# Optimization experiments

Measured on AMD Instinct MI355X. Metric: run time of the kernel, lower is better.

Reference implementation:

```python
import jax, jax.numpy as jnp
import numpy as np

LS = (0, 2, 4, 6, 8)
L_IN, L_OUT, SYM = 8, 8, 2
A, B, N, C = 2, 2, 1024, 8  # ti_n, te_n, voxels, b_out

def _triples():
    out = []
    for l in range(0, L_OUT + 1, SYM):
        for l1 in range(0, L_IN + 1, SYM):
            for l2 in range(l1, L_IN + 1, SYM):
                if abs(l2 - l1) <= l <= l1 + l2:
                    out.append((l, l1, l2))
    return tuple(out)

TRIPLES = _triples()
# Clebsch-Gordan-like constants (fixed random; same structural shapes as the real CG tables)
_rng = np.random.RandomState(42)
CG_R = {t: jnp.asarray((_rng.randn(2 * t[0] + 1, 2 * t[1] + 1, 2 * t[2] + 1) * 0.1).astype(np.float32)) for t in TRIPLES}
CG_L = {t: jnp.asarray((_rng.randn(2 * t[0] + 1, 2 * t[2] + 1, 2 * t[1] + 1) * 0.1).astype(np.float32)) for t in TRIPLES}


def setup_inputs() -> dict:
    key = jax.random.key(0)
    ks = jax.random.split(key, 11)
    inp = {}
    for i, l in enumerate(LS):
        i_l = 5 if l == 0 else 2
        inp[f"x{l}"] = jax.random.normal(ks[i], (A, B, N, i_l, 2 * l + 1), dtype=jnp.float32)
        inp[f"w{l}"] = jax.random.uniform(ks[5 + i], (A, B, i_l, C, 2 * l + 1), dtype=jnp.float32) * 0.1
    inp["bias"] = jnp.zeros((A, B, 1, C, 1, 1), dtype=jnp.float32)
    return inp


def _forward(x0, x2, x4, x6, x8, w0, w2, w4, w6, w8, bias):
    xs = {0: x0, 2: x2, 4: x4, 6: x6, 8: x8}
    ws = {0: w0, 2: w2, 4: w4, 6: w6, 8: w8}
    # spectral convolution: rh[l] = x[l] @ w[l], shape (a,b,n,c,2l+1,2l+1)
    rh = {}
    for l in LS:
        r = jnp.einsum('abnil,abiok->abnolk', xs[l], ws[l])
        if l == 0:
            r = r + bias
        rh[l] = r
    # CG tensor-product quadratic nonlinearity
    rh_n = {}
    for (l, l1, l2) in TRIPLES:
        a, b, n, c = rh[l1].shape[:4]
        xx = jnp.einsum('abncij,klj->abnckli', rh[l2], CG_R[(l, l1, l2)])
        xx = xx.reshape(a, b, n, c, 2 * l + 1, -1)  # flat dim = (2l1+1)*(2l2+1)
        yy = jnp.einsum('abncji,klj->abnckil', rh[l1], CG_L[(l, l1, l2)])
        yy = yy.reshape(a, b, n, c, 2 * l + 1, -1)
        z = jnp.einsum('abncki,abncji->abnckj', yy, xx)  # (a,b,n,c,2l+1,2l+1)
        rh_n[l] = z if l not in rh_n else rh_n[l] + z
    # power-spectrum features
    feats = []
    for l in LS:
        n_l = np.float32(8.0 * np.pi ** 2 / (2 * l + 1))
        f = jnp.sum(rh_n[l] ** 2, axis=(4, 5)).reshape(A, B, -1)  # (a,b,n*c)
        feats.append(n_l * f)
    feats = jnp.concatenate(feats, axis=2)  # (a,b, 5*n*c)
    return feats, rh_n


def reference(x0, x2, x4, x6, x8, w0, w2, w4, w6, w8, bias):
    feats, rh_n = _forward(x0, x2, x4, x6, x8, w0, w2, w4, w6, w8, bias)
    return (feats, rh_n[0], rh_n[2], rh_n[4], rh_n[6], rh_n[8])
```

## Files before the change

kernel.cpp:

```cpp
#include <hip/hip_runtime.h>
#include <cmath>
#include <cstdint>
#include <vector>
#include <cstdlib>
#include <algorithm>

#define WGB 256

typedef float vf4 __attribute__((ext_vector_type(4)));

struct TripleMeta { int l,l1,l2,d,d1,d2,form,dp4,cgR,cgL,uv; };
struct AllMeta { TripleMeta t[48]; int nT, cgTotal, uvTotal; };

constexpr AllMeta build_meta() {
  AllMeta M{};
  const int LSl[5] = {0,2,4,6,8};
  int k=0, cg=0;
  for (int a=0;a<5;a++){ const int l=LSl[a];
    for (int b=0;b<5;b++){ const int l1=LSl[b];
      for (int l2=l1;l2<=8;l2+=2){
        if (!((l2-l1)<=l && l<=(l1+l2))) continue;
        TripleMeta m{};
        m.l=l; m.l1=l1; m.l2=l2;
        m.d=2*l+1; m.d1=2*l1+1; m.d2=2*l2+1;
        m.form = (l1==0) ? ((l2==0)?2:1) : 0;
        m.dp4 = ((m.d+3)/4)*4;
        m.cgR = cg; cg += m.d*m.d1*m.d2;
        M.t[k] = m; k++;
      } } }
  M.nT=k; M.cgTotal=cg;
  int cgl=cg;
  for (int i=0;i<k;i++){ M.t[i].cgL=cgl; cgl += M.t[i].d*M.t[i].d1*M.t[i].d2; }
  int uv=0;
  for (int i=0;i<k;i++){
    if (M.t[i].form==0){ M.t[i].uv=uv; uv += 4*M.t[i].dp4; }
    else if (M.t[i].form==1){ M.t[i].uv=uv; uv += 2*M.t[i].dp4; }
  }
  M.uvTotal=uv;
  return M;
}

constexpr AllMeta META_H = build_meta();
static_assert(META_H.nT==42, "nT");
static_assert(META_H.cgTotal==52334, "cgTotal");
static_assert(META_H.uvTotal==2048, "uvTotal");

__device__ constexpr AllMeta META = build_meta();

constexpr int CG_TOTAL  = 52334;
constexpr int UVS       = 2048;
constexpr int ZTOT      = 4520;
constexpr int NUC       = 417;
constexpr int XBS       = 104;

__device__ constexpr int DL[5]     = {1,5,9,13,17};
__device__ constexpr int T0G[6]    = {0,5,13,23,33,42};
__device__ constexpr int RHNB[5]   = {163840,196608,1015808,3670016,9207808};
__device__ constexpr int CBASE[5]  = {352,312,240,136,0};
__device__ constexpr int ZB[5]     = {0,8,208,856,2208};
__device__ constexpr int LEN5[5]   = {8,200,648,1352,2312};
__device__ constexpr int C4[6]     = {0,2,52,214,552,1130};

__global__ __launch_bounds__(128) void s2_prep(
    const float* __restrict__ w2, const float* __restrict__ w4,
    const float* __restrict__ w6, const float* __restrict__ w8,
    const float* __restrict__ cg, float* __restrict__ V)
{
  __shared__ float Rs[4928];
  const int bid = blockIdx.x;
  const int t   = bid >> 5;
  const int abc = bid & 31;
  const auto &m = META.t[t];
  if (m.form == 2) return;
  const int ab = abc >> 3, c = abc & 7;
  const int sz = m.d * m.d1 * m.d2;
  for (int i = threadIdx.x; i < sz; i += 128) Rs[i] = cg[m.cgR + i];
  __syncthreads();
  const float* ws[4] = {w2,w4,w6,w8};
  const int nout = (m.form==0 ? 4 : 2) * m.d;
  if ((int)threadIdx.x < nout){
    const int pq = threadIdx.x / m.d;
    const int k2 = threadIdx.x - pq*m.d;
    float s = 0.f;
    if (m.form==0){
      const int p = pq>>1, q = pq&1;
      const float* wA = ws[(m.l1>>1)-1] + ((ab*2+p)*8 + c)*m.d1;
      const float* wB = ws[(m.l2>>1)-1] + ((ab*2+q)*8 + c)*m.d2;
      const float* Rk = Rs + k2*m.d1*m.d2;
      for (int a=0;a<m.d1;a++){
        float t2 = 0.f;
        for (int j=0;j<m.d2;j++) t2 += wB[j]*Rk[a*m.d2+j];
        s += wA[a]*t2;
      }
    } else {
      const float* wB = ws[(m.l2>>1)-1] + ((ab*2+pq)*8 + c)*m.d2;
      const float* Rk = Rs + k2*m.d2;
      for (int j=0;j<m.d2;j++) s += wB[j]*Rk[j];
    }
    V[abc*UVS + m.uv + pq*m.dp4 + k2] = s;
  }
}

template<int D1>
__device__ __forceinline__ void u_itemA(const float* __restrict__ Lp, const float* xb,
    float* Ush, int dst, int dstr, int xo1, int xo2, int d2)
{
  float x0r[2*D1], x1r[2*D1];
  #pragma unroll
  for (int j=0;j<2*D1;j++){ x0r[j] = xb[xo1+j]; x1r[j] = xb[XBS+xo1+j]; }
  float a00=0.f,a01=0.f,a10=0.f,a11=0.f;
  float b00=0.f,b01=0.f,b10=0.f,b11=0.f;
  for (int b=0;b<d2;b++){
    float i00=0.f, i01=0.f, i10=0.f, i11=0.f;
    const float* Lb = Lp + b*D1;
    #pragma unroll
    for (int j=0;j<D1;j++){
      const float lv=Lb[j];
      i00+=lv*x0r[j]; i01+=lv*x0r[D1+j];
      i10+=lv*x1r[j]; i11+=lv*x1r[D1+j];
    }
    const float q00=xb[xo2+b],     q01=xb[xo2+d2+b];
    const float q10=xb[XBS+xo2+b], q11=xb[XBS+xo2+d2+b];
    a00+=q00*i00; a01+=q01*i00; a10+=q00*i01; a11+=q01*i01;
    b00+=q10*i10; b01+=q11*i10; b10+=q10*i11; b11+=q11*i11;
  }
  Ush[dst]=a00; Ush[dst+dstr]=a01; Ush[dst+2*dstr]=a10; Ush[dst+3*dstr]=a11;
  Ush[UVS+dst]=b00; Ush[UVS+dst+dstr]=b01; Ush[UVS+dst+2*dstr]=b10; Ush[UVS+dst+3*dstr]=b11;
}

__device__ __forceinline__ void u_item(const int4 w, const float* __restrict__ cg,
                                       const float* xb, float* Ush)
{
  const float* Lp = cg + w.x;
  const int dst = w.y & 0xFFFF, dstr = ((unsigned)w.y) >> 16;
  const int xo1 = w.z & 0xFF, xo2 = (w.z>>8)&0xFF;
  const int d1 = (w.z>>16)&0x3F, d2 = ((unsigned)w.z)>>22;
  if (d1 == 0){
    float a0=0.f, a1=0.f, b0=0.f, b1=0.f;
    for (int b=0;b<d2;b++){
      const float lv=Lp[b];
      a0+=lv*xb[xo2+b];     a1+=lv*xb[xo2+d2+b];
      b0+=lv*xb[XBS+xo2+b]; b1+=lv*xb[XBS+xo2+d2+b];
    }
    Ush[dst]=a0; Ush[dst+dstr]=a1;
    Ush[UVS+dst]=b0; Ush[UVS+dst+dstr]=b1;
    return;
  }
  switch(d1){
    case 5:  u_itemA<5>(Lp,xb,Ush,dst,dstr,xo1,xo2,d2); break;
    case 9:  u_itemA<9>(Lp,xb,Ush,dst,dstr,xo1,xo2,d2); break;
    case 13: u_itemA<13>(Lp,xb,Ush,dst,dstr,xo1,xo2,d2); break;
    default: u_itemA<17>(Lp,xb,Ush,dst,dstr,xo1,xo2,d2); break;
  }
}

template<int LI>
__device__ __forceinline__ float col_work(int k2, float rh0c, float c000,
    const float* __restrict__ Vc, const float* Ush,
    float* zsh, int zb)
{
  constexpr int d   = (LI==0)?1:(LI==1)?5:(LI==2)?9:(LI==3)?13:17;
  constexpr int np4 = (d+3)/4;
  float4 za[np4];
  #pragma unroll
  for (int i=0;i<np4;i++) za[i] = make_float4(0.f,0.f,0.f,0.f);
  #pragma unroll
  for (int t=T0G[LI]; t<T0G[LI+1]; t++){
    const auto &m = META.t[t];
    if (m.form==2){
      za[0].x += rh0c*rh0c*c000;
    } else {
      const int npr = (m.form==0)?4:2;
      #pragma unroll
      for (int pr=0;pr<npr;pr++){
        float v = Vc[m.uv + pr*m.dp4 + k2];
        if (m.form==1) v *= rh0c;
        const float4* Up = reinterpret_cast<const float4*>(Ush + m.uv + pr*m.dp4);
        #pragma unroll
        for (int rr=0;rr<np4;rr++){
          float4 u = Up[rr];
          za[rr].x += u.x*v; za[rr].y += u.y*v; za[rr].z += u.z*v; za[rr].w += u.w*v;
        }
      }
    }
  }
  float s = 0.f;
  #pragma unroll
  for (int rr=0;rr<np4;rr++){
    const float vals[4] = {za[rr].x, za[rr].y, za[rr].z, za[rr].w};
    #pragma unroll
    for (int e=0;e<4;e++){
      const int k1 = 4*rr+e;
      if (k1 < d){
        zsh[zb + k1*d + k2] = vals[e];
        s += vals[e]*vals[e];
      }
    }
  }
  return s;
}

__global__ __launch_bounds__(WGB,4) void s2_main(
    const float* __restrict__ x0, const float* __restrict__ x2, const float* __restrict__ x4,
    const float* __restrict__ x6, const float* __restrict__ x8,
    const float* __restrict__ w0, const float* __restrict__ bias,
    const float* __restrict__ cg, const int4* __restrict__ wiU,
    const float* __restrict__ V, float* __restrict__ out, float c000)
{
  __shared__ alignas(16) float SH[ZTOT + 2*UVS];
  __shared__ float xb[2*XBS];
  __shared__ float rh0s[16];
  __shared__ float fpart[360];
  const int tid = threadIdx.x;
  const int bid = blockIdx.x;
  const int ab  = bid >> 9;
  float* Ush = SH + ZTOT;

  {
    const int v  = tid >> 7;
    const int t2 = tid & 127;
    const int vox = bid*2 + v;
    float* xv = xb + v*XBS;
    if (t2 < 5)        xv[t2]           = x0[vox*5  + t2];
    else if (t2 < 15)  xv[8  + (t2-5)]  = x2[vox*10 + (t2-5)];
    else if (t2 < 33)  xv[18 + (t2-15)] = x4[vox*18 + (t2-15)];
    else if (t2 < 59)  xv[36 + (t2-33)] = x6[vox*26 + (t2-33)];
    else if (t2 < 93)  xv[62 + (t2-59)] = x8[vox*34 + (t2-59)];
    else if (t2 >= 96 && t2 < 104) {
      const int c = t2 - 96;
      float s = bias[ab*8 + c];
      for (int i=0;i<5;i++) s += x0[vox*5+i] * w0[(ab*5+i)*8 + c];
      rh0s[v*8 + c] = s;
    }
  }
  __syncthreads();

  u_item(wiU[tid], cg, xb, Ush);
  {
    const int r = NUC-1-tid;
    if (r >= WGB) u_item(wiU[r], cg, xb, Ush);
  }
  __syncthreads();

  const float* Vab = V + (ab*8)*UVS;
  #pragma unroll
  for (int v=0; v<2; v++){
    const int bid2 = bid*2 + v;
    const float* Uv = Ush + v*UVS;
    for (int col=tid; col<360; col+=WGB){
      int li, c, k2;
      if (col < 136)      { li=4; c = col/17;            k2 = col - c*17; }
      else if (col < 240) { const int r=col-136; li=3; c=r/13; k2=r-c*13; }
      else if (col < 312) { const int r=col-240; li=2; c=r/9;  k2=r-c*9;  }
      else if (col < 352) { const int r=col-312; li=1; c=r/5;  k2=r-c*5;  }
      else                { li=0; c=col-352; k2=0; }
      const int d = DL[li];
      const float rh0c = rh0s[v*8 + c];
      const float* Vc = Vab + c*UVS;
      const int zb = ZB[li] + c*d*d;
      float s;
      switch(li){
        case 4:  s = col_work<4>(k2, rh0c, c000, Vc, Uv, SH, zb); break;
        case 3:  s = col_work<3>(k2, rh0c, c000, Vc, Uv, SH, zb); break;
        case 2:  s = col_work<2>(k2, rh0c, c000, Vc, Uv, SH, zb); break;
        case 1:  s = col_work<1>(k2, rh0c, c000, Vc, Uv, SH, zb); break;
        default: s = col_work<0>(k2, rh0c, c000, Vc, Uv, SH, zb); break;
      }
      fpart[col] = s;
    }
    __syncthreads();

    for (int i4 = tid; i4 < 1130; i4 += WGB){
      int li;
      if      (i4 < C4[1]) li = 0;
      else if (i4 < C4[2]) li = 1;
      else if (i4 < C4[3]) li = 2;
      else if (i4 < C4[4]) li = 3;
      else                 li = 4;
      const int r4 = i4 - C4[li];
      const vf4 zv = *reinterpret_cast<const vf4*>(SH + ZB[li] + 4*r4);
      __builtin_nontemporal_store(zv, reinterpret_cast<vf4*>(out + RHNB[li] + bid2*LEN5[li] + 4*r4));
    }

    if (tid < 40){
      const int li = tid >> 3, c = tid & 7;
      const int d = DL[li];
      float s = 0.f;
      for (int k2=0;k2<d;k2++) s += fpart[CBASE[li] + c*d + k2];
      const double nl_d = 8.0*3.14159265358979323846*3.14159265358979323846/(double)(2*(2*li)+1);
      const int n = bid2 & 1023;
      __builtin_nontemporal_store((float)nl_d * s, out + ab*40960 + li*8192 + n*8 + c);
    }
    if (v==0) __syncthreads();
  }
}

namespace {

struct MTRng {
  uint32_t mt[624]; int mti;
  bool has_g; double g;
  void seed(uint32_t s){
    for (int pos=0; pos<624; pos++){ mt[pos]=s; s = 1812433253u*(s^(s>>30)) + (uint32_t)pos + 1u; }
    mti = 624; has_g=false; g=0.0;
  }
  uint32_t next32(){
    if (mti >= 624){
      for (int i=0;i<624;i++){
        uint32_t y = (mt[i]&0x80000000u) | (mt[(i+1)%624]&0x7fffffffu);
        mt[i] = mt[(i+397)%624] ^ (y>>1) ^ ((y&1u) ? 0x9908b0dfu : 0u);
      }
      mti = 0;
    }
    uint32_t y = mt[mti++];
    y ^= y>>11; y ^= (y<<7)&0x9d2c5680u; y ^= (y<<15)&0xefc60000u; y ^= y>>18;
    return y;
  }
  double rk_double(){
    uint32_t a = next32()>>5, b = next32()>>6;
    return (a*67108864.0 + b)/9007199254740992.0;
  }
  double gauss(){
    if (has_g){ has_g=false; return g; }
    double f,x1,x2,r2;
    do {
      x1 = 2.0*rk_double()-1.0;
      x2 = 2.0*rk_double()-1.0;
      r2 = x1*x1 + x2*x2;
    } while (r2 >= 1.0 || r2 == 0.0);
    f = std::sqrt(-2.0*std::log(r2)/r2);
    g = f*x1; has_g = true;
    return f*x2;
  }
};

constexpr int XOFS_H[5] = {0,8,18,36,62};

struct DeviceSetup {
  float* d_cg  = nullptr;
  float* d_v   = nullptr;
  int4*  d_wiU = nullptr;
  float  c000  = 0.f;
  DeviceSetup(){
    std::vector<float> h(2*CG_TOTAL);
    MTRng r; r.seed(42u);
    for (int i=0;i<2*CG_TOTAL;i++) h[i] = (float)(r.gauss()*0.1);
    c000 = h[META_H.t[0].cgL] * h[META_H.t[0].cgR];

    std::vector<std::pair<int,int4>> tmp;
    for (int t=0;t<META_H.nT;t++){
      const TripleMeta &m = META_H.t[t];
      if (m.form==0){
        const int xo1 = XOFS_H[m.l1>>1], xo2 = XOFS_H[m.l2>>1];
        for (int k1=0;k1<m.d;k1++){
          int4 e;
          e.x = m.cgL + k1*m.d1*m.d2;
          e.y = (m.uv + k1) | (m.dp4<<16);
          e.z = xo1 | (xo2<<8) | (m.d1<<16) | (m.d2<<22);
          e.w = 0;
          tmp.push_back({m.d2*(2*m.d1+4), e});
        }
      } else if (m.form==1){
        const int xo2 = XOFS_H[m.l2>>1];
        for (int k1=0;k1<m.d;k1++){
          int4 e;
          e.x = m.cgL + k1*m.d2;
          e.y = (m.uv + k1) | (m.dp4<<16);
          e.z = (xo2<<8) | (0<<16) | (m.d2<<22);
          e.w = 0;
          tmp.push_back({2*m.d2, e});
        }
      }
    }
    if ((int)tmp.size() != NUC) std::abort();
    std::stable_sort(tmp.begin(), tmp.end(),
                     [](const std::pair<int,int4>&a, const std::pair<int,int4>&b){
                       return a.first > b.first; });
    std::vector<int4> wiU(NUC);
    for (int i=0;i<NUC;i++) wiU[i] = tmp[i].second;

    (void)hipMalloc((void**)&d_cg,  sizeof(float)*2*CG_TOTAL);
    (void)hipMalloc((void**)&d_v,   sizeof(float)*32*UVS);
    (void)hipMalloc((void**)&d_wiU, sizeof(int4)*NUC);
    (void)hipMemcpy(d_cg,  h.data(),    sizeof(float)*2*CG_TOTAL, hipMemcpyHostToDevice);
    (void)hipMemcpy(d_wiU, wiU.data(),  sizeof(int4)*NUC,  hipMemcpyHostToDevice);
  }
};
DeviceSetup g_dev;

}

extern "C" void kernel_launch(void* const* d_in, const int* in_sizes, int n_in,
                              void* d_out, int out_size, void* d_ws, size_t ws_size,
                              hipStream_t stream)
{
  (void)in_sizes; (void)n_in; (void)d_ws; (void)ws_size; (void)out_size;
  const float* x0   = (const float*)d_in[0];
  const float* w0   = (const float*)d_in[1];
  const float* x2   = (const float*)d_in[2];
  const float* w2   = (const float*)d_in[3];
  const float* x4   = (const float*)d_in[4];
  const float* w4   = (const float*)d_in[5];
  const float* x6   = (const float*)d_in[6];
  const float* w6   = (const float*)d_in[7];
  const float* x8   = (const float*)d_in[8];
  const float* w8   = (const float*)d_in[9];
  const float* bias = (const float*)d_in[10];
  float* out = (float*)d_out;

  s2_prep<<<dim3(42*32), dim3(128), 0, stream>>>(w2,w4,w6,w8, g_dev.d_cg, g_dev.d_v);
  s2_main<<<dim3(2048), dim3(WGB), 0, stream>>>(x0,x2,x4,x6,x8, w0, bias,
                                                g_dev.d_cg, g_dev.d_wiU,
                                                g_dev.d_v, out, g_dev.c000);
}
```

Measured before the change: 249.1 us.

## Drop LDS staging of z, schedule per-wave work by degree, regroup prep blocks

The main kernel no longer stages the rh_n output tiles in shared memory. Each thread now writes its z column straight to global memory with nontemporal stores, and the two voxel passes and their barriers are merged into one. Cutting the LDS footprint allows the launch bound to rise to 8 workgroups per CU. Column work and U-item work are assigned to waves through static, degree-grouped schedules so each wave runs a single template instantiation and stays uniform. The prep kernel is also reorganised into 84 blocks of 512 threads instead of 1344 small blocks. The trade-off is that the strided scalar global stores are less coalesced than the earlier vectorised float4 stores from shared memory.

```diff
diff --git a/kernel.cpp b/kernel.cpp
--- a/kernel.cpp
+++ b/kernel.cpp
@@ -6,8 +6,6 @@
 #include <algorithm>
 
 #define WGB 256
-
-typedef float vf4 __attribute__((ext_vector_type(4)));
 
 struct TripleMeta { int l,l1,l2,d,d1,d2,form,dp4,cgR,cgL,uv; };
 struct AllMeta { TripleMeta t[48]; int nT, cgTotal, uvTotal; };
@@ -49,38 +47,46 @@
 
 constexpr int CG_TOTAL  = 52334;
 constexpr int UVS       = 2048;
-constexpr int ZTOT      = 4520;
-constexpr int NUC       = 417;
 constexpr int XBS       = 104;
+constexpr int WI_N      = 512;
 
 __device__ constexpr int DL[5]     = {1,5,9,13,17};
 __device__ constexpr int T0G[6]    = {0,5,13,23,33,42};
 __device__ constexpr int RHNB[5]   = {163840,196608,1015808,3670016,9207808};
 __device__ constexpr int CBASE[5]  = {352,312,240,136,0};
-__device__ constexpr int ZB[5]     = {0,8,208,856,2208};
 __device__ constexpr int LEN5[5]   = {8,200,648,1352,2312};
-__device__ constexpr int C4[6]     = {0,2,52,214,552,1130};
-
-__global__ __launch_bounds__(128) void s2_prep(
+
+__device__ constexpr int SCHED3[4][5][2] = {
+  {{4,0},{4,64},{3,0},{-1,0},{-1,0}},
+  {{4,128},{4,192},{3,64},{-1,0},{-1,0}},
+  {{4,256},{3,128},{2,0},{1,0},{-1,0}},
+  {{3,192},{2,64},{2,128},{1,64},{0,0}},
+};
+
+__global__ __launch_bounds__(512) void s2_prep(
     const float* __restrict__ w2, const float* __restrict__ w4,
     const float* __restrict__ w6, const float* __restrict__ w8,
     const float* __restrict__ cg, float* __restrict__ V)
 {
   __shared__ float Rs[4928];
-  const int bid = blockIdx.x;
-  const int t   = bid >> 5;
-  const int abc = bid & 31;
+  const int t    = blockIdx.x >> 1;
+  const int half = blockIdx.x & 1;
   const auto &m = META.t[t];
   if (m.form == 2) return;
-  const int ab = abc >> 3, c = abc & 7;
   const int sz = m.d * m.d1 * m.d2;
-  for (int i = threadIdx.x; i < sz; i += 128) Rs[i] = cg[m.cgR + i];
+  for (int i = threadIdx.x; i < sz; i += 512) Rs[i] = cg[m.cgR + i];
   __syncthreads();
   const float* ws[4] = {w2,w4,w6,w8};
-  const int nout = (m.form==0 ? 4 : 2) * m.d;
-  if ((int)threadIdx.x < nout){
-    const int pq = threadIdx.x / m.d;
-    const int k2 = threadIdx.x - pq*m.d;
+  const int npq  = (m.form==0) ? 4 : 2;
+  const int nout = npq * m.d;
+  const int tot  = 16 * nout;
+  for (int idx = threadIdx.x; idx < tot; idx += 512){
+    const int al  = idx / nout;
+    const int rem = idx - al*nout;
+    const int abc = half*16 + al;
+    const int ab = abc >> 3, c = abc & 7;
+    const int pq = rem / m.d;
+    const int k2 = rem - pq*m.d;
     float s = 0.f;
     if (m.form==0){
       const int p = pq>>1, q = pq&1;
@@ -131,6 +137,7 @@
 __device__ __forceinline__ void u_item(const int4 w, const float* __restrict__ cg,
                                        const float* xb, float* Ush)
 {
+  if (w.z == 0) return;
   const float* Lp = cg + w.x;
   const int dst = w.y & 0xFFFF, dstr = ((unsigned)w.y) >> 16;
   const int xo1 = w.z & 0xFF, xo2 = (w.z>>8)&0xFF;
@@ -156,10 +163,9 @@
 
 template<int LI>
 __device__ __forceinline__ float col_work(int k2, float rh0c, float c000,
-    const float* __restrict__ Vc, const float* Ush,
-    float* zsh, int zb)
-{
-  constexpr int d   = (LI==0)?1:(LI==1)?5:(LI==2)?9:(LI==3)?13:17;
+    const float* __restrict__ Vc, const float* Ush, float* __restrict__ zg)
+{
+  constexpr int d   = 4*LI + 1;
   constexpr int np4 = (d+3)/4;
   float4 za[np4];
   #pragma unroll
@@ -192,7 +198,7 @@
     for (int e=0;e<4;e++){
       const int k1 = 4*rr+e;
       if (k1 < d){
-        zsh[zb + k1*d + k2] = vals[e];
+        __builtin_nontemporal_store(vals[e], zg + k1*d);
         s += vals[e]*vals[e];
       }
     }
@@ -200,21 +206,38 @@
   return s;
 }
 
-__global__ __launch_bounds__(WGB,4) void s2_main(
+template<int LI>
+__device__ __forceinline__ void do_pass(int base, int lane, int bid,
+    const float* __restrict__ Vab, const float* Ush, const float* rh0s,
+    float* fpart, float* __restrict__ out, float c000)
+{
+  constexpr int d = 4*LI + 1;
+  const int col = base + lane;
+  if (col >= 16*d) return;
+  const int v  = (col >= 8*d) ? 1 : 0;
+  const int r  = col - v*8*d;
+  const int c  = r / d;
+  const int k2 = r - c*d;
+  float* zg = out + RHNB[LI] + (bid*2+v)*LEN5[LI] + c*(d*d) + k2;
+  const float s = col_work<LI>(k2, rh0s[v*8+c], c000, Vab + c*UVS, Ush + v*UVS, zg);
+  fpart[v*360 + CBASE[LI] + c*d + k2] = s;
+}
+
+__global__ __launch_bounds__(WGB,8) void s2_main(
     const float* __restrict__ x0, const float* __restrict__ x2, const float* __restrict__ x4,
     const float* __restrict__ x6, const float* __restrict__ x8,
     const float* __restrict__ w0, const float* __restrict__ bias,
     const float* __restrict__ cg, const int4* __restrict__ wiU,
     const float* __restrict__ V, float* __restrict__ out, float c000)
 {
-  __shared__ alignas(16) float SH[ZTOT + 2*UVS];
-  __shared__ float xb[2*XBS];
-  __shared__ float rh0s[16];
-  __shared__ float fpart[360];
+  __shared__ alignas(16) float SH[2*UVS + 2*XBS + 16 + 720];
+  float* const Ush   = SH;
+  float* const xb    = SH + 2*UVS;
+  float* const rh0s  = SH + 2*UVS + 2*XBS;
+  float* const fpart = SH + 2*UVS + 2*XBS + 16;
   const int tid = threadIdx.x;
   const int bid = blockIdx.x;
   const int ab  = bid >> 9;
-  float* Ush = SH + ZTOT;
 
   {
     const int v  = tid >> 7;
@@ -235,63 +258,38 @@
   }
   __syncthreads();
 
-  u_item(wiU[tid], cg, xb, Ush);
-  {
-    const int r = NUC-1-tid;
-    if (r >= WGB) u_item(wiU[r], cg, xb, Ush);
-  }
+  #pragma unroll 1
+  for (int it=0; it<2; it++) u_item(wiU[it*WGB + tid], cg, xb, Ush);
   __syncthreads();
 
   const float* Vab = V + (ab*8)*UVS;
-  #pragma unroll
-  for (int v=0; v<2; v++){
+  const int wid = tid>>6, lane = tid&63;
+  #pragma unroll 1
+  for (int pi=0; pi<5; pi++){
+    const int li = SCHED3[wid][pi][0];
+    if (li < 0) break;
+    const int base = SCHED3[wid][pi][1];
+    switch(li){
+      case 4:  do_pass<4>(base,lane,bid,Vab,Ush,rh0s,fpart,out,c000); break;
+      case 3:  do_pass<3>(base,lane,bid,Vab,Ush,rh0s,fpart,out,c000); break;
+      case 2:  do_pass<2>(base,lane,bid,Vab,Ush,rh0s,fpart,out,c000); break;
+      case 1:  do_pass<1>(base,lane,bid,Vab,Ush,rh0s,fpart,out,c000); break;
+      default: do_pass<0>(base,lane,bid,Vab,Ush,rh0s,fpart,out,c000); break;
+    }
+  }
+  __syncthreads();
+
+  if (tid < 80){
+    const int v  = (tid >= 40) ? 1 : 0;
+    const int r  = tid - v*40;
+    const int li = r >> 3, c = r & 7;
+    const int d = DL[li];
+    float s = 0.f;
+    for (int k2=0;k2<d;k2++) s += fpart[v*360 + CBASE[li] + c*d + k2];
+    const double nl_d = 8.0*3.14159265358979323846*3.14159265358979323846/(double)(2*(2*li)+1);
     const int bid2 = bid*2 + v;
-    const float* Uv = Ush + v*UVS;
-    for (int col=tid; col<360; col+=WGB){
-      int li, c, k2;
-      if (col < 136)      { li=4; c = col/17;            k2 = col - c*17; }
-      else if (col < 240) { const int r=col-136; li=3; c=r/13; k2=r-c*13; }
-      else if (col < 312) { const int r=col-240; li=2; c=r/9;  k2=r-c*9;  }
-      else if (col < 352) { const int r=col-312; li=1; c=r/5;  k2=r-c*5;  }
-      else                { li=0; c=col-352; k2=0; }
-      const int d = DL[li];
-      const float rh0c = rh0s[v*8 + c];
-      const float* Vc = Vab + c*UVS;
-      const int zb = ZB[li] + c*d*d;
-      float s;
-      switch(li){
-        case 4:  s = col_work<4>(k2, rh0c, c000, Vc, Uv, SH, zb); break;
-        case 3:  s = col_work<3>(k2, rh0c, c000, Vc, Uv, SH, zb); break;
-        case 2:  s = col_work<2>(k2, rh0c, c000, Vc, Uv, SH, zb); break;
-        case 1:  s = col_work<1>(k2, rh0c, c000, Vc, Uv, SH, zb); break;
-        default: s = col_work<0>(k2, rh0c, c000, Vc, Uv, SH, zb); break;
-      }
-      fpart[col] = s;
-    }
-    __syncthreads();
-
-    for (int i4 = tid; i4 < 1130; i4 += WGB){
-      int li;
-      if      (i4 < C4[1]) li = 0;
-      else if (i4 < C4[2]) li = 1;
-      else if (i4 < C4[3]) li = 2;
-      else if (i4 < C4[4]) li = 3;
-      else                 li = 4;
-      const int r4 = i4 - C4[li];
-      const vf4 zv = *reinterpret_cast<const vf4*>(SH + ZB[li] + 4*r4);
-      __builtin_nontemporal_store(zv, reinterpret_cast<vf4*>(out + RHNB[li] + bid2*LEN5[li] + 4*r4));
-    }
-
-    if (tid < 40){
-      const int li = tid >> 3, c = tid & 7;
-      const int d = DL[li];
-      float s = 0.f;
-      for (int k2=0;k2<d;k2++) s += fpart[CBASE[li] + c*d + k2];
-      const double nl_d = 8.0*3.14159265358979323846*3.14159265358979323846/(double)(2*(2*li)+1);
-      const int n = bid2 & 1023;
-      __builtin_nontemporal_store((float)nl_d * s, out + ab*40960 + li*8192 + n*8 + c);
-    }
-    if (v==0) __syncthreads();
+    const int n = bid2 & 1023;
+    __builtin_nontemporal_store((float)nl_d * s, out + ab*40960 + li*8192 + n*8 + c);
   }
 }
 
@@ -347,7 +345,8 @@
     for (int i=0;i<2*CG_TOTAL;i++) h[i] = (float)(r.gauss()*0.1);
     c000 = h[META_H.t[0].cgL] * h[META_H.t[0].cgR];
 
-    std::vector<std::pair<int,int4>> tmp;
+    struct HItem { int d2; int4 e; };
+    std::vector<HItem> grp[5];
     for (int t=0;t<META_H.nT;t++){
       const TripleMeta &m = META_H.t[t];
       if (m.form==0){
@@ -358,7 +357,7 @@
           e.y = (m.uv + k1) | (m.dp4<<16);
           e.z = xo1 | (xo2<<8) | (m.d1<<16) | (m.d2<<22);
           e.w = 0;
-          tmp.push_back({m.d2*(2*m.d1+4), e});
+          grp[(m.l1>>1)-1].push_back({m.d2, e});
         }
       } else if (m.form==1){
         const int xo2 = XOFS_H[m.l2>>1];
@@ -368,22 +367,35 @@
           e.y = (m.uv + k1) | (m.dp4<<16);
           e.z = (xo2<<8) | (0<<16) | (m.d2<<22);
           e.w = 0;
-          tmp.push_back({2*m.d2, e});
+          grp[4].push_back({m.d2, e});
         }
       }
     }
-    if ((int)tmp.size() != NUC) std::abort();
-    std::stable_sort(tmp.begin(), tmp.end(),
-                     [](const std::pair<int,int4>&a, const std::pair<int,int4>&b){
-                       return a.first > b.first; });
-    std::vector<int4> wiU(NUC);
-    for (int i=0;i<NUC;i++) wiU[i] = tmp[i].second;
+    if (grp[0].size()!=111 || grp[1].size()!=128 || grp[2].size()!=89 ||
+        grp[3].size()!=45  || grp[4].size()!=44) std::abort();
+    for (int g=0; g<5; g++)
+      std::stable_sort(grp[g].begin(), grp[g].end(),
+                       [](const HItem&a, const HItem&b){ return a.d2 > b.d2; });
+
+    int4 zero; zero.x=0; zero.y=0; zero.z=0; zero.w=0;
+    std::vector<int4> wiU(WI_N, zero);
+    auto place = [&](int iter, int w, const std::vector<HItem>& g, int s, int n){
+      for (int i=0;i<n;i++) wiU[iter*256 + w*64 + i] = g[s+i].e;
+    };
+    place(0,0,grp[3],0,45);
+    place(0,1,grp[2],0,64);
+    place(0,2,grp[2],64,25);
+    place(0,3,grp[1],0,64);
+    place(1,0,grp[4],0,44);
+    place(1,1,grp[0],64,47);
+    place(1,2,grp[1],64,64);
+    place(1,3,grp[0],0,64);
 
     (void)hipMalloc((void**)&d_cg,  sizeof(float)*2*CG_TOTAL);
     (void)hipMalloc((void**)&d_v,   sizeof(float)*32*UVS);
-    (void)hipMalloc((void**)&d_wiU, sizeof(int4)*NUC);
+    (void)hipMalloc((void**)&d_wiU, sizeof(int4)*WI_N);
     (void)hipMemcpy(d_cg,  h.data(),    sizeof(float)*2*CG_TOTAL, hipMemcpyHostToDevice);
-    (void)hipMemcpy(d_wiU, wiU.data(),  sizeof(int4)*NUC,  hipMemcpyHostToDevice);
+    (void)hipMemcpy(d_wiU, wiU.data(),  sizeof(int4)*WI_N,  hipMemcpyHostToDevice);
   }
 };
 DeviceSetup g_dev;
@@ -408,7 +420,7 @@
   const float* bias = (const float*)d_in[10];
   float* out = (float*)d_out;
 
-  s2_prep<<<dim3(42*32), dim3(128), 0, stream>>>(w2,w4,w6,w8, g_dev.d_cg, g_dev.d_v);
+  s2_prep<<<dim3(42*2), dim3(512), 0, stream>>>(w2,w4,w6,w8, g_dev.d_cg, g_dev.d_v);
   s2_main<<<dim3(2048), dim3(WGB), 0, stream>>>(x0,x2,x4,x6,x8, w0, bias,
                                                 g_dev.d_cg, g_dev.d_wiU,
                                                 g_dev.d_v, out, g_dev.c000);
```

New measurement: 629.9 us. 2.53x slower.
